# Performance work log

Measured on AMD Instinct MI355X. Metric: run time of the kernel, lower is better.

## Reference

```python
import jax, jax.numpy as jnp
import numpy as np

NEG_BIG = 1e8  # diagonal mask penalty from the original code


def setup_inputs() -> dict:
    key = jax.random.key(0)
    ks = jax.random.split(key, 8)
    B, N, E, H, D, Hm = 2, 1024, 256, 64, 64, 128
    return {
        "encoder_output": jax.random.normal(ks[0], (B, N, E), dtype=jnp.float32),
        "wl": jax.random.normal(ks[1], (E, H), dtype=jnp.float32) * (1.0 / np.sqrt(E)),
        "wr": jax.random.normal(ks[2], (E, H), dtype=jnp.float32) * (1.0 / np.sqrt(E)),
        "u": jax.random.normal(ks[3], (H,), dtype=jnp.float32) * (1.0 / np.sqrt(H)),
        "l_bias": jnp.zeros((1,), dtype=jnp.float32),
        "edge_query": jax.random.normal(ks[4], (N, D), dtype=jnp.float32),
        "mlp_w1": jax.random.normal(ks[5], (D, Hm), dtype=jnp.float32) * (1.0 / np.sqrt(D)),
        "mlp_b1": jnp.zeros((Hm,), dtype=jnp.float32),
        "mlp_w2": jax.random.normal(ks[6], (Hm, 1), dtype=jnp.float32) * (1.0 / np.sqrt(Hm)),
        "mlp_b2": jnp.zeros((1,), dtype=jnp.float32),
    }


def reference(encoder_output, wl, wr, u, l_bias, edge_query, mlp_w1, mlp_b1, mlp_w2, mlp_b2):
    # edge-weight MLP: [E_edges, d] -> [E_edges]
    w_logits = (jax.nn.relu(edge_query @ mlp_w1 + mlp_b1) @ mlp_w2 + mlp_b2)[:, 0]
    w = jax.nn.softplus(w_logits) + 1e-8

    # pairwise additive attention logits
    dot_l = jnp.einsum("bne,eh->bnh", encoder_output, wl)  # [B,N,H]
    dot_r = jnp.einsum("bne,eh->bnh", encoder_output, wr)  # [B,N,H]
    final_sum = jnp.tanh(dot_l[:, :, None, :] + dot_r[:, None, :, :])  # [B,N,N,H]
    logits = jnp.einsum("bijh,h->bij", final_sum, u) + l_bias[0]  # [B,N,N]

    # vectorized diagonal masking (replaces the per-node python loop)
    N = logits.shape[1]
    eye = jnp.eye(N, dtype=logits.dtype)
    mask_scores = logits - NEG_BIG * eye[None, :, :]  # [B,N,N]

    probs = jax.nn.sigmoid(mask_scores)
    samples = (jax.random.uniform(jax.random.key(1), mask_scores.shape) < probs).astype(logits.dtype)
    # Bernoulli entropy from logits: softplus(l) - l * sigmoid(l)
    entropy = jax.nn.softplus(mask_scores) - mask_scores * probs
    return samples, mask_scores, entropy, w
```

## Files before the change

kernel.cpp:

```cpp
#include <hip/hip_runtime.h>
#include <hip/hip_bf16.h>


#define L2E 1.4426950408889634f
#define C2  2.8853900817779268f
#define LN2 0.6931471805599453f
#define RCP(x) __builtin_amdgcn_rcpf(x)
#define EXP2(x) __builtin_amdgcn_exp2f(x)
#define LOG2(x) __builtin_amdgcn_logf(x)

__device__ __forceinline__ void threefry2x32_01(unsigned x0, unsigned x1,
                                                unsigned& o0, unsigned& o1) {
  const unsigned k0 = 0u, k1 = 1u;
  const unsigned k2 = 0x1BD11BDAu ^ k0 ^ k1;
#define TF_R(r) { x0 += x1; x1 = (x1 << r) | (x1 >> (32 - r)); x1 ^= x0; }
  x0 += k0; x1 += k1;
  TF_R(13) TF_R(15) TF_R(26) TF_R(6)
  x0 += k1; x1 += k2 + 1u;
  TF_R(17) TF_R(29) TF_R(16) TF_R(24)
  x0 += k2; x1 += k0 + 2u;
  TF_R(13) TF_R(15) TF_R(26) TF_R(6)
  x0 += k0; x1 += k1 + 3u;
  TF_R(17) TF_R(29) TF_R(16) TF_R(24)
  x0 += k1; x1 += k2 + 4u;
  TF_R(13) TF_R(15) TF_R(26) TF_R(6)
  x0 += k2; x1 += k0 + 5u;
#undef TF_R
  o0 = x0; o1 = x1;
}

__device__ __forceinline__ float tf_uniform(unsigned y) {
  return __uint_as_float((y >> 9) | 0x3f800000u) - 1.0f;
}

__global__ __launch_bounds__(256) void prep_kernel(
    const float* __restrict__ enc, const float* __restrict__ wl,
    const float* __restrict__ wr, float* __restrict__ ws,
    const float* __restrict__ eq, const float* __restrict__ w1,
    const float* __restrict__ b1, const float* __restrict__ w2,
    const float* __restrict__ b2, float* __restrict__ wout) {
  __shared__ float As[32][33];
  __shared__ float Ws[32][34];
  __shared__ float eql[2][64];
  __shared__ float part[4];
  const int t = threadIdx.x;
  const int bx = blockIdx.x;

  if (bx < 256) {
    const int r0 = (bx & 63) * 32;
    const int c0 = (bx >> 6) * 32;
    const float* __restrict__ wmat = (c0 < 64) ? wl : wr;
    const int cbase = c0 & 63;
    const int ty = t >> 4, tx = t & 15;
    float acc[2][2] = {};
    for (int ec = 0; ec < 8; ++ec) {
      {
        const int rr = t >> 3, e4 = (t & 7) * 4;
        const float4 v = *(const float4*)(enc + (r0 + rr) * 256 + ec * 32 + e4);
        As[rr][e4] = v.x; As[rr][e4 + 1] = v.y; As[rr][e4 + 2] = v.z; As[rr][e4 + 3] = v.w;
        const float4 w = *(const float4*)(wmat + (ec * 32 + rr) * 64 + cbase + e4);
        Ws[rr][e4] = w.x; Ws[rr][e4 + 1] = w.y; Ws[rr][e4 + 2] = w.z; Ws[rr][e4 + 3] = w.w;
      }
      __syncthreads();
#pragma unroll
      for (int e = 0; e < 32; ++e) {
        const float a0 = As[2 * ty][e];
        const float a1 = As[2 * ty + 1][e];
        const float2 wv = *(const float2*)&Ws[e][2 * tx];
        acc[0][0] = fmaf(a0, wv.x, acc[0][0]);
        acc[0][1] = fmaf(a0, wv.y, acc[0][1]);
        acc[1][0] = fmaf(a1, wv.x, acc[1][0]);
        acc[1][1] = fmaf(a1, wv.y, acc[1][1]);
      }
      __syncthreads();
    }
    const int matoff = (c0 < 64) ? 0 : 131072;
#pragma unroll
    for (int i = 0; i < 2; ++i) {
      const int r = r0 + 2 * ty + i;
      const int b = r >> 10, n = r & 1023;
#pragma unroll
      for (int j = 0; j < 2; ++j) {
        const int c = cbase + 2 * tx + j;
        ws[matoff + b * 65536 + c * 1024 + n] = EXP2(C2 * acc[i][j]);
      }
    }
  } else {
    const int row = t >> 7;
    const int e = (bx - 256) * 2 + row;
    const int h = t & 127;
    if (h < 64) eql[row][h] = eq[e * 64 + h];
    __syncthreads();
    float acc = b1[h];
#pragma unroll 8
    for (int k = 0; k < 64; ++k) acc = fmaf(eql[row][k], w1[k * 128 + h], acc);
    float v = fmaxf(acc, 0.0f) * w2[h];
#pragma unroll
    for (int off = 32; off > 0; off >>= 1) v += __shfl_down(v, off);
    if ((t & 63) == 0) part[t >> 6] = v;
    __syncthreads();
    if (h == 0) {
      const float l = part[row * 2] + part[row * 2 + 1] + b2[0];
      const float sp = fmaxf(l, 0.0f) + log1pf(expf(-fabsf(l)));
      wout[e] = sp + 1e-8f;
    }
  }
}

__global__ __launch_bounds__(256) void pair_kernel(
    const float* __restrict__ ws, const float* __restrict__ u,
    const float* __restrict__ lb, float* __restrict__ out) {
  __shared__ float sA[64 * 32];
  __shared__ float sB[64 * 64];
  __shared__ float sU[64];
  const int t = threadIdx.x;
  const int b = blockIdx.z;
  const int i0 = blockIdx.x * 32;
  const int j0 = blockIdx.y * 64;
  const float* __restrict__ srcA = ws + b * 65536;
  const float* __restrict__ srcB = ws + 131072 + b * 65536;

  {
    const int h = t >> 3, c = (t & 7) * 4;
    *(float4*)(sA + h * 32 + c) = *(const float4*)(srcA + h * 1024 + i0 + c);
    *(float4*)(sA + (h + 32) * 32 + c) =
        *(const float4*)(srcA + (h + 32) * 1024 + i0 + c);
  }
  {
    const int h = t >> 4, c = (t & 15) * 4;
#pragma unroll
    for (int q = 0; q < 4; ++q)
      *(float4*)(sB + (h + 16 * q) * 64 + c) =
          *(const float4*)(srcB + (h + 16 * q) * 1024 + j0 + c);
  }
  if (t < 64) sU[t] = u[t];
  __syncthreads();

  const int ia = (t >> 4) * 2;
  const int ja = (t & 15) * 4;
  float acc[2][4] = {};
#pragma unroll
  for (int h4 = 0; h4 < 16; ++h4) {
    const float4 uc = *(const float4*)(sU + h4 * 4);
#pragma unroll
    for (int hh = 0; hh < 4; ++hh) {
      const int h = h4 * 4 + hh;
      const float uh = (&uc.x)[hh];
      const float2 av = *(const float2*)(sA + h * 32 + ia);
      const float4 bv = *(const float4*)(sB + h * 64 + ja);
      const float a[2] = {av.x, av.y};
      const float bb[4] = {bv.x, bv.y, bv.z, bv.w};
#pragma unroll
      for (int ii = 0; ii < 2; ++ii)
#pragma unroll
        for (int jj = 0; jj < 4; ++jj)
          acc[ii][jj] = fmaf(uh, RCP(fmaf(a[ii], bb[jj], 1.0f)), acc[ii][jj]);
    }
  }

  float uv = sU[t & 63];
#pragma unroll
  for (int off = 32; off > 0; off >>= 1) uv += __shfl_xor(uv, off);
  const float su = uv + lb[0];

  float* __restrict__ outS = out + b * 1048576;
  float* __restrict__ outM = out + 2097152 + b * 1048576;
  float* __restrict__ outE = out + 4194304 + b * 1048576;
#pragma unroll
  for (int ii = 0; ii < 2; ++ii) {
    const int gi = i0 + ia + ii;
    const unsigned mb = (unsigned)(gi * 1024 + j0 + ja);
    float4 sv, ev, smv;
#pragma unroll
    for (int jj = 0; jj < 4; ++jj) {
      const int gj = j0 + ja + jj;
      unsigned y0, y1;
      threefry2x32_01(mb + (unsigned)jj, mb + (unsigned)jj + 1048576u, y0, y1);
      const float uu = tf_uniform(b ? y1 : y0);
      float s = fmaf(-2.0f, acc[ii][jj], su);
      if (gi == gj) s -= 1e8f;
      const float ex = EXP2(-s * L2E);
      const float p = RCP(1.0f + ex);
      const float em = EXP2(-fabsf(s) * L2E);
      const float ent = fmaxf(s, 0.0f) + LOG2(1.0f + em) * LN2 - s * p;
      (&sv.x)[jj] = s;
      (&ev.x)[jj] = ent;
      (&smv.x)[jj] = (uu < p) ? 1.0f : 0.0f;
    }
    const int base = gi * 1024 + j0 + ja;
    *(float4*)(outS + base) = smv;
    *(float4*)(outM + base) = sv;
    *(float4*)(outE + base) = ev;
  }
}

extern "C" void kernel_launch(void* const* d_in, const int* in_sizes, int n_in,
                              void* d_out, int out_size, void* d_ws, size_t ws_size,
                              hipStream_t stream) {
  const float* enc = (const float*)d_in[0];
  const float* wl  = (const float*)d_in[1];
  const float* wr  = (const float*)d_in[2];
  const float* u   = (const float*)d_in[3];
  const float* lb  = (const float*)d_in[4];
  const float* eq  = (const float*)d_in[5];
  const float* w1  = (const float*)d_in[6];
  const float* b1  = (const float*)d_in[7];
  const float* w2  = (const float*)d_in[8];
  const float* b2  = (const float*)d_in[9];
  float* out = (float*)d_out;
  float* wsf = (float*)d_ws;

  prep_kernel<<<768, 256, 0, stream>>>(enc, wl, wr, wsf, eq, w1, b1, w2, b2,
                                       out + 6291456);
  pair_kernel<<<dim3(32, 16, 2), 256, 0, stream>>>(wsf, u, lb, out);
}
```

Before: 108.9 us.

## Fuse prep and pair stages into one cooperative kernel with grid sync

Merges the projection/MLP prep kernel and the pairwise logits kernel into a single cooperative launch of 512 blocks. A grid-wide barrier separates the stages, and each block then handles two pair tiles. The MLP stage is reworked so each block handles 4 rows using 64-lane halves. This removes one kernel launch and the gap between launches, at the cost of grid-sync overhead and a fixed 512-block grid that may reduce latency hiding in the pair stage. If the cooperative launch fails, it falls back to the original two-kernel launch.

Result: slower. 180.1 us (+65.4%).

```diff
diff --git a/kernel.cpp b/kernel.cpp
--- a/kernel.cpp
+++ b/kernel.cpp
@@ -1,5 +1,8 @@
 #include <hip/hip_runtime.h>
 #include <hip/hip_bf16.h>
+#include <hip/hip_cooperative_groups.h>
+
+namespace cg = cooperative_groups;
 
 
 #define L2E 1.4426950408889634f
@@ -33,90 +36,64 @@
   return __uint_as_float((y >> 9) | 0x3f800000u) - 1.0f;
 }
 
-__global__ __launch_bounds__(256) void prep_kernel(
-    const float* __restrict__ enc, const float* __restrict__ wl,
-    const float* __restrict__ wr, float* __restrict__ ws,
-    const float* __restrict__ eq, const float* __restrict__ w1,
-    const float* __restrict__ b1, const float* __restrict__ w2,
-    const float* __restrict__ b2, float* __restrict__ wout) {
-  __shared__ float As[32][33];
-  __shared__ float Ws[32][34];
-  __shared__ float eql[2][64];
-  __shared__ float part[4];
-  const int t = threadIdx.x;
-  const int bx = blockIdx.x;
-
-  if (bx < 256) {
-    const int r0 = (bx & 63) * 32;
-    const int c0 = (bx >> 6) * 32;
-    const float* __restrict__ wmat = (c0 < 64) ? wl : wr;
-    const int cbase = c0 & 63;
-    const int ty = t >> 4, tx = t & 15;
-    float acc[2][2] = {};
-    for (int ec = 0; ec < 8; ++ec) {
-      {
-        const int rr = t >> 3, e4 = (t & 7) * 4;
-        const float4 v = *(const float4*)(enc + (r0 + rr) * 256 + ec * 32 + e4);
-        As[rr][e4] = v.x; As[rr][e4 + 1] = v.y; As[rr][e4 + 2] = v.z; As[rr][e4 + 3] = v.w;
-        const float4 w = *(const float4*)(wmat + (ec * 32 + rr) * 64 + cbase + e4);
-        Ws[rr][e4] = w.x; Ws[rr][e4 + 1] = w.y; Ws[rr][e4 + 2] = w.z; Ws[rr][e4 + 3] = w.w;
-      }
-      __syncthreads();
-#pragma unroll
-      for (int e = 0; e < 32; ++e) {
-        const float a0 = As[2 * ty][e];
-        const float a1 = As[2 * ty + 1][e];
-        const float2 wv = *(const float2*)&Ws[e][2 * tx];
-        acc[0][0] = fmaf(a0, wv.x, acc[0][0]);
-        acc[0][1] = fmaf(a0, wv.y, acc[0][1]);
-        acc[1][0] = fmaf(a1, wv.x, acc[1][0]);
-        acc[1][1] = fmaf(a1, wv.y, acc[1][1]);
-      }
-      __syncthreads();
-    }
-    const int matoff = (c0 < 64) ? 0 : 131072;
-#pragma unroll
-    for (int i = 0; i < 2; ++i) {
-      const int r = r0 + 2 * ty + i;
-      const int b = r >> 10, n = r & 1023;
-#pragma unroll
-      for (int j = 0; j < 2; ++j) {
-        const int c = cbase + 2 * tx + j;
-        ws[matoff + b * 65536 + c * 1024 + n] = EXP2(C2 * acc[i][j]);
-      }
-    }
-  } else {
-    const int row = t >> 7;
-    const int e = (bx - 256) * 2 + row;
-    const int h = t & 127;
-    if (h < 64) eql[row][h] = eq[e * 64 + h];
+__device__ __forceinline__ void proj_tile(
+    float* lds, int t, int tileid, const float* __restrict__ enc,
+    const float* __restrict__ wl, const float* __restrict__ wr,
+    float* __restrict__ ws) {
+  float* As = lds;
+  float* Ws = lds + 1056;
+  const int r0 = (tileid & 63) * 32;
+  const int c0 = (tileid >> 6) * 32;
+  const float* __restrict__ wmat = (c0 < 64) ? wl : wr;
+  const int cbase = c0 & 63;
+  const int ty = t >> 4, tx = t & 15;
+  float acc[2][2] = {};
+  for (int ec = 0; ec < 8; ++ec) {
+    {
+      const int rr = t >> 3, e4 = (t & 7) * 4;
+      const float4 v = *(const float4*)(enc + (r0 + rr) * 256 + ec * 32 + e4);
+      As[rr * 33 + e4] = v.x; As[rr * 33 + e4 + 1] = v.y;
+      As[rr * 33 + e4 + 2] = v.z; As[rr * 33 + e4 + 3] = v.w;
+      const float4 w = *(const float4*)(wmat + (ec * 32 + rr) * 64 + cbase + e4);
+      Ws[rr * 34 + e4] = w.x; Ws[rr * 34 + e4 + 1] = w.y;
+      Ws[rr * 34 + e4 + 2] = w.z; Ws[rr * 34 + e4 + 3] = w.w;
+    }
     __syncthreads();
-    float acc = b1[h];
-#pragma unroll 8
-    for (int k = 0; k < 64; ++k) acc = fmaf(eql[row][k], w1[k * 128 + h], acc);
-    float v = fmaxf(acc, 0.0f) * w2[h];
-#pragma unroll
-    for (int off = 32; off > 0; off >>= 1) v += __shfl_down(v, off);
-    if ((t & 63) == 0) part[t >> 6] = v;
+#pragma unroll
+    for (int e = 0; e < 32; ++e) {
+      const float a0 = As[(2 * ty) * 33 + e];
+      const float a1 = As[(2 * ty + 1) * 33 + e];
+      const float2 wv = *(const float2*)&Ws[e * 34 + 2 * tx];
+      acc[0][0] = fmaf(a0, wv.x, acc[0][0]);
+      acc[0][1] = fmaf(a0, wv.y, acc[0][1]);
+      acc[1][0] = fmaf(a1, wv.x, acc[1][0]);
+      acc[1][1] = fmaf(a1, wv.y, acc[1][1]);
+    }
     __syncthreads();
-    if (h == 0) {
-      const float l = part[row * 2] + part[row * 2 + 1] + b2[0];
-      const float sp = fmaxf(l, 0.0f) + log1pf(expf(-fabsf(l)));
-      wout[e] = sp + 1e-8f;
-    }
-  }
-}
-
-__global__ __launch_bounds__(256) void pair_kernel(
-    const float* __restrict__ ws, const float* __restrict__ u,
-    const float* __restrict__ lb, float* __restrict__ out) {
-  __shared__ float sA[64 * 32];
-  __shared__ float sB[64 * 64];
-  __shared__ float sU[64];
-  const int t = threadIdx.x;
-  const int b = blockIdx.z;
-  const int i0 = blockIdx.x * 32;
-  const int j0 = blockIdx.y * 64;
+  }
+  const int matoff = (c0 < 64) ? 0 : 131072;
+#pragma unroll
+  for (int i = 0; i < 2; ++i) {
+    const int r = r0 + 2 * ty + i;
+    const int b = r >> 10, n = r & 1023;
+#pragma unroll
+    for (int j = 0; j < 2; ++j) {
+      const int c = cbase + 2 * tx + j;
+      ws[matoff + b * 65536 + c * 1024 + n] = EXP2(C2 * acc[i][j]);
+    }
+  }
+}
+
+__device__ __forceinline__ void pair_tile(
+    float* lds, int t, int T, const float* __restrict__ ws,
+    const float* __restrict__ u, const float* __restrict__ lb,
+    float* __restrict__ out) {
+  float* sA = lds;
+  float* sB = lds + 2048;
+  float* sU = lds + 6144;
+  const int b = T >> 9;
+  const int i0 = (T & 31) * 32;
+  const int j0 = ((T >> 5) & 15) * 64;
   const float* __restrict__ srcA = ws + b * 65536;
   const float* __restrict__ srcB = ws + 131072 + b * 65536;
 
@@ -192,6 +169,83 @@
     *(float4*)(outM + base) = sv;
     *(float4*)(outE + base) = ev;
   }
+}
+
+__device__ __forceinline__ void mlp_rows(
+    float* lds, int t, int e0, const float* __restrict__ eq,
+    const float* __restrict__ w1, const float* __restrict__ b1,
+    const float* __restrict__ w2, const float* __restrict__ b2,
+    float* __restrict__ wout) {
+  float* eql = lds;
+  const int row = t >> 6, lane = t & 63;
+  const int e = e0 + row;
+  eql[row * 64 + lane] = eq[e * 64 + lane];
+  __syncthreads();
+  float acc0 = b1[lane], acc1 = b1[lane + 64];
+#pragma unroll 8
+  for (int k = 0; k < 64; ++k) {
+    const float ev = eql[row * 64 + k];
+    acc0 = fmaf(ev, w1[k * 128 + lane], acc0);
+    acc1 = fmaf(ev, w1[k * 128 + 64 + lane], acc1);
+  }
+  float v = fmaxf(acc0, 0.0f) * w2[lane] + fmaxf(acc1, 0.0f) * w2[lane + 64];
+#pragma unroll
+  for (int off = 32; off > 0; off >>= 1) v += __shfl_xor(v, off);
+  if (lane == 0) {
+    const float l = v + b2[0];
+    const float sp = fmaxf(l, 0.0f) + log1pf(expf(-fabsf(l)));
+    wout[e] = sp + 1e-8f;
+  }
+}
+
+__global__ __launch_bounds__(256, 2) void fused_kernel(
+    const float* __restrict__ enc, const float* __restrict__ wl,
+    const float* __restrict__ wr, float* __restrict__ ws,
+    const float* __restrict__ eq, const float* __restrict__ w1,
+    const float* __restrict__ b1, const float* __restrict__ w2,
+    const float* __restrict__ b2, const float* __restrict__ u,
+    const float* __restrict__ lb, float* __restrict__ out) {
+  __shared__ float lds[6208];
+  const int t = threadIdx.x;
+  const int bx = blockIdx.x;
+
+  if (bx < 256) {
+    proj_tile(lds, t, bx, enc, wl, wr, ws);
+  } else {
+    mlp_rows(lds, t, (bx - 256) * 4, eq, w1, b1, w2, b2, out + 6291456);
+  }
+
+  cg::this_grid().sync();
+
+#pragma unroll
+  for (int k = 0; k < 2; ++k) {
+    __syncthreads();
+    pair_tile(lds, t, bx + 512 * k, ws, u, lb, out);
+  }
+}
+
+__global__ __launch_bounds__(256) void prep_kernel(
+    const float* __restrict__ enc, const float* __restrict__ wl,
+    const float* __restrict__ wr, float* __restrict__ ws,
+    const float* __restrict__ eq, const float* __restrict__ w1,
+    const float* __restrict__ b1, const float* __restrict__ w2,
+    const float* __restrict__ b2, float* __restrict__ wout) {
+  __shared__ float lds[2144];
+  const int t = threadIdx.x;
+  const int bx = blockIdx.x;
+  if (bx < 256) {
+    proj_tile(lds, t, bx, enc, wl, wr, ws);
+  } else {
+    mlp_rows(lds, t, (bx - 256) * 4, eq, w1, b1, w2, b2, wout);
+  }
+}
+
+__global__ __launch_bounds__(256) void pair_kernel(
+    const float* __restrict__ ws, const float* __restrict__ u,
+    const float* __restrict__ lb, float* __restrict__ out) {
+  __shared__ float lds[6208];
+  const int T = blockIdx.x + (blockIdx.y << 5) + (blockIdx.z << 9);
+  pair_tile(lds, threadIdx.x, T, ws, u, lb, out);
 }
 
 extern "C" void kernel_launch(void* const* d_in, const int* in_sizes, int n_in,
@@ -210,7 +264,15 @@
   float* out = (float*)d_out;
   float* wsf = (float*)d_ws;
 
-  prep_kernel<<<768, 256, 0, stream>>>(enc, wl, wr, wsf, eq, w1, b1, w2, b2,
-                                       out + 6291456);
-  pair_kernel<<<dim3(32, 16, 2), 256, 0, stream>>>(wsf, u, lb, out);
-}
+  void* args[] = {(void*)&enc, (void*)&wl, (void*)&wr, (void*)&wsf,
+                  (void*)&eq,  (void*)&w1, (void*)&b1, (void*)&w2,
+                  (void*)&b2,  (void*)&u,  (void*)&lb, (void*)&out};
+  hipError_t rc = hipLaunchCooperativeKernel((const void*)fused_kernel,
+                                             dim3(512), dim3(256), args, 0,
+                                             stream);
+  if (rc != hipSuccess) {
+    prep_kernel<<<320, 256, 0, stream>>>(enc, wl, wr, wsf, eq, w1, b1, w2, b2,
+                                         out + 6291456);
+    pair_kernel<<<dim3(32, 16, 2), 256, 0, stream>>>(wsf, u, lb, out);
+  }
+}
```
